# Kernel tuning notes

Measured on AMD Instinct MI355X. Metric: run time of the kernel, lower is better.

The kernel has to match this reference:

```python
import jax, jax.numpy as jnp
import numpy as np

B, T = 128, 2048
E, OUT, HID = 8, 32, 64          # num_experts, kan_out_features, gru_hidden_dim
GRID_SIZE, ORDER = 5, 3          # standard efficient-kan defaults
KCOEF = GRID_SIZE + ORDER        # B-spline basis functions per input feature


def make_grid():
    # extended knot grid on [-1, 1], length GRID_SIZE + 2*ORDER + 1
    h = 2.0 / GRID_SIZE
    return jnp.arange(-ORDER, GRID_SIZE + ORDER + 1, dtype=jnp.float32) * h - 1.0


def b_splines(x, grid):
    # x: [..., in_features] -> [..., in_features, KCOEF] via Cox-de Boor recursion
    x = x[..., None]
    b = ((x >= grid[:-1]) & (x < grid[1:])).astype(x.dtype)
    for k in range(1, ORDER + 1):
        left = (x - grid[:-(k + 1)]) / (grid[k:-1] - grid[:-(k + 1)])
        right = (grid[k + 1:] - x) / (grid[k + 1:] - grid[1:-k])
        b = left * b[..., :-1] + right * b[..., 1:]
    return b


def kan_moe(x, gate_w, gate_b, base_w, spline_w, grid):
    # x: [B,T,in=1]; dense softmax-gated mixture of KANLinear experts
    gate = jax.nn.softmax(x @ gate_w + gate_b, axis=-1)                 # [B,T,E]
    base_out = jnp.einsum('bti,eoi->bteo', jax.nn.silu(x), base_w)      # [B,T,E,OUT]
    bs = b_splines(x, grid).reshape(x.shape[0], x.shape[1], -1)         # [B,T,in*KCOEF]
    spline_out = jnp.einsum('btk,eok->bteo', bs, spline_w)              # [B,T,E,OUT]
    return jnp.einsum('bte,bteo->bto', gate, base_out + spline_out)     # [B,T,OUT]


def gru(x, w_ih, w_hh, b_ih, b_hh):
    # PyTorch GRU convention: gates ordered (r, z, n); batch_first semantics
    xp = jnp.einsum('btf,gf->btg', x, w_ih) + b_ih                      # [B,T,3H]

    def step(h, xt):
        hp = h @ w_hh.T + b_hh
        xr, xz, xn = jnp.split(xt, 3, axis=-1)
        hr, hz, hn = jnp.split(hp, 3, axis=-1)
        r = jax.nn.sigmoid(xr + hr)
        z = jax.nn.sigmoid(xz + hz)
        n = jnp.tanh(xn + r * hn)
        h = (1.0 - z) * n + z * h
        return h, h

    h0 = jnp.zeros((x.shape[0], HID), x.dtype)
    _, hs = jax.lax.scan(step, h0, jnp.swapaxes(xp, 0, 1))
    return jnp.swapaxes(hs, 0, 1)                                       # [B,T,H]


def setup_inputs() -> dict:
    key = jax.random.key(0)
    ks = jax.random.split(key, 12)
    def n(k, shape, scale=0.1):
        return jax.random.normal(k, shape, jnp.float32) * scale
    return {
        'a': jax.random.normal(ks[0], (B, T, 1), jnp.float32),
        'd': jax.random.normal(ks[1], (B, T, 1), jnp.float32),
        'gate_w_a': n(ks[2], (1, E)), 'gate_b_a': jnp.zeros((E,), jnp.float32),
        'base_w_a': n(ks[3], (E, OUT, 1)), 'spline_w_a': n(ks[4], (E, OUT, KCOEF)),
        'gate_w_d': n(ks[5], (1, E)), 'gate_b_d': jnp.zeros((E,), jnp.float32),
        'base_w_d': n(ks[6], (E, OUT, 1)), 'spline_w_d': n(ks[7], (E, OUT, KCOEF)),
        'conv_w': n(ks[8], (OUT, OUT, 5)), 'conv_b': jnp.zeros((OUT,), jnp.float32),
        'w_ih': n(ks[9], (3 * HID, OUT)), 'w_hh': n(ks[10], (3 * HID, HID)),
        'b_ih': jnp.zeros((3 * HID,), jnp.float32), 'b_hh': jnp.zeros((3 * HID,), jnp.float32),
    }


def reference(a, d, gate_w_a, gate_b_a, base_w_a, spline_w_a,
              gate_w_d, gate_b_d, base_w_d, spline_w_d,
              conv_w, conv_b, w_ih, w_hh, b_ih, b_hh):
    grid = make_grid()
    fa = kan_moe(a, gate_w_a, gate_b_a, base_w_a, spline_w_a, grid)     # trend features
    fd = kan_moe(d, gate_w_d, gate_b_d, base_w_d, spline_w_d, grid)     # residual features
    # TemporalBlock: permute -> Conv1d(padding='same') -> ReLU -> permute back
    xc = jnp.swapaxes(fa, 1, 2)                                         # [B,C,T]
    yc = jax.lax.conv_general_dilated(
        xc, conv_w, (1,), 'SAME', dimension_numbers=('NCH', 'OIH', 'NCH')
    ) + conv_b[None, :, None]
    trend = jnp.swapaxes(jax.nn.relu(yc), 1, 2)                         # [B,T,OUT]
    ctx = gru(fd, w_ih, w_hh, b_ih, b_hh)                               # [B,T,HID]
    # dropout is identity in eval mode
    return jnp.concatenate([trend, ctx], axis=-1)                       # [B,T,OUT+HID]
```

## Files before the change

kernel.cpp:

```cpp
#include <hip/hip_runtime.h>
#include <cstdint>

typedef _Float16 half2_t __attribute__((ext_vector_type(2)));

#define B_   128
#define T_   2048
#define E_   8
#define OUT_ 32
#define HID_ 64
#define KC_  8
#define TILE_A 128
#define NSEG 4
#define SEGT (T_ / NSEG)
#define WUPC 4
#define CH_  32

__device__ __forceinline__ float frcp(float x) { return __builtin_amdgcn_rcpf(x); }
__device__ __forceinline__ float exp2_(float x) {
#if __has_builtin(__builtin_amdgcn_exp2f)
  return __builtin_amdgcn_exp2f(x);
#else
  return exp2f(x);
#endif
}
__device__ __forceinline__ float fsig(float x) { return frcp(1.0f + __expf(-x)); }

__device__ __forceinline__ float fdot2_(half2_t a, half2_t b, float c) {
#if __has_builtin(__builtin_amdgcn_fdot2)
  return __builtin_amdgcn_fdot2(a, b, c, false);
#else
  return fmaf((float)a.x, (float)b.x, fmaf((float)a.y, (float)b.y, c));
#endif
}

__device__ __forceinline__ half2_t u2h2(unsigned u) {
  return __builtin_bit_cast(half2_t, u);
}
__device__ __forceinline__ half2_t packh2(float a, float b) {
  half2_t h; h.x = (_Float16)a; h.y = (_Float16)b; return h;
}
__device__ __forceinline__ float rlanef(float v, int i) {
  return __int_as_float(__builtin_amdgcn_readlane(__float_as_int(v), i));
}
__device__ __forceinline__ unsigned rlaneu(unsigned v, int i) {
  return (unsigned)__builtin_amdgcn_readlane((int)v, i);
}

#define NLOG2E  (-1.4426950408889634f)
#define N2LOG2E (-2.8853900817779268f)

__device__ __forceinline__ void kan_scalars(float x, const float* gwr, const float* gbr,
                                            float& silu, float* gate, float* bs) {
  silu = x * fsig(x);
  float le[E_];
  float m = -1e30f;
#pragma unroll
  for (int e = 0; e < E_; ++e) { le[e] = fmaf(x, gwr[e], gbr[e]); m = fmaxf(m, le[e]); }
  float s = 0.f;
#pragma unroll
  for (int e = 0; e < E_; ++e) { gate[e] = __expf(le[e] - m); s += gate[e]; }
  float inv = frcp(s);
#pragma unroll
  for (int e = 0; e < E_; ++e) gate[e] *= inv;
  float g[12];
#pragma unroll
  for (int i = 0; i < 12; ++i) g[i] = (float)(i - 3) * 0.4f - 1.0f;
  float bb[11];
#pragma unroll
  for (int i = 0; i < 11; ++i) bb[i] = (x >= g[i] && x < g[i + 1]) ? 1.0f : 0.0f;
#pragma unroll
  for (int k = 1; k <= 3; ++k) {
#pragma unroll
    for (int i = 0; i < 11 - k; ++i) {
      const float dl = 1.0f / (g[i + k] - g[i]);
      const float dr = 1.0f / (g[i + k + 1] - g[i + 1]);
      float left  = (x - g[i]) * dl;
      float right = (g[i + k + 1] - x) * dr;
      bb[i] = left * bb[i] + right * bb[i + 1];
    }
  }
#pragma unroll
  for (int i = 0; i < KC_; ++i) bs[i] = bb[i];
}

__global__ __launch_bounds__(256, 1) void fused3_kernel(
    const float* __restrict__ a, const float* __restrict__ d,
    const float* __restrict__ gwa, const float* __restrict__ gba,
    const float* __restrict__ bwa, const float* __restrict__ swa,
    const float* __restrict__ gwd, const float* __restrict__ gbd,
    const float* __restrict__ bwd, const float* __restrict__ swd,
    const float* __restrict__ cw, const float* __restrict__ cb,
    const float* __restrict__ wih_g, const float* __restrict__ whh_g,
    const float* __restrict__ bih_g, const float* __restrict__ bhh_g,
    float* __restrict__ out)
{
  __shared__ __align__(16) char smem_[47360];
  const int tid = threadIdx.x;

  if (blockIdx.x < NSEG * B_) {
    auto xqc = (uint2 (*)[CH_][64])smem_;
    auto hbc = (unsigned short*)(smem_ + 32768);

    const int bid = (int)blockIdx.x;
    const int b = bid & (B_ - 1);
    const int seg = bid >> 7;
    const int tstart = (seg == 0) ? 0 : (seg * SEGT - WUPC * CH_);
    const int wup = (seg == 0) ? 0 : WUPC;
    const int nch = ((seg == 0) ? SEGT : (SEGT + WUPC * CH_)) / CH_;
    const int w = tid >> 6;
    const int role = (w - (bid & 3)) & 3;
    const int ln = tid & 63;
    const size_t db = (size_t)b * T_;
    float* outrow = out + db * 96 + 32;
    const uint4* hq4 = (const uint4*)hbc;

    half2_t whhp[3][32];
    float bhh3[3];
    uint4 u0, u1, u2, u3, u4, u5, u6, u7;
    if (role == 0) {
#pragma unroll
      for (int g3 = 0; g3 < 3; ++g3) {
        const float sc = (g3 == 2) ? N2LOG2E : NLOG2E;
        const int g = g3 * 64 + ln;
#pragma unroll
        for (int i = 0; i < 64; i += 4) {
          const float4 v = *(const float4*)&whh_g[(size_t)g * 64 + i];
          whhp[g3][i / 2]     = packh2(v.x * sc, v.y * sc);
          whhp[g3][i / 2 + 1] = packh2(v.z * sc, v.w * sc);
        }
        bhh3[g3] = bhh_g[g] * sc;
      }
      hbc[ln] = __builtin_bit_cast(unsigned short, (_Float16)0.0f);
      asm volatile("" ::: "memory");
      u0 = hq4[0]; u1 = hq4[1]; u2 = hq4[2]; u3 = hq4[3];
      u4 = hq4[4]; u5 = hq4[5]; u6 = hq4[6]; u7 = hq4[7];
    }

    float A_[E_];
    half2_t Beh[E_][4];
    float bihr = 0.f;
    float gwrd[E_], gbrd[E_];
    const int p3 = (role >= 1) ? (role - 1) : 0;
    if (role >= 1) {
      const float sc = (p3 == 2) ? N2LOG2E : NLOG2E;
      const int g = p3 * 64 + ln;
      float wihr[32];
#pragma unroll
      for (int i = 0; i < 32; i += 4) {
        float4 v = *(const float4*)&wih_g[(size_t)g * 32 + i];
        wihr[i] = v.x * sc; wihr[i + 1] = v.y * sc;
        wihr[i + 2] = v.z * sc; wihr[i + 3] = v.w * sc;
      }
      bihr = bih_g[g] * sc;
#pragma unroll
      for (int e = 0; e < E_; ++e) { gwrd[e] = gwd[e]; gbrd[e] = gbd[e]; }
#pragma unroll
      for (int e = 0; e < E_; ++e) {
        float acc = 0.f;
#pragma unroll 4
        for (int c = 0; c < 32; c += 4) {
          const float4 bv = *(const float4*)&bwd[e * OUT_ + c];
          acc = fmaf(wihr[c], bv.x, acc);
          acc = fmaf(wihr[c + 1], bv.y, acc);
          acc = fmaf(wihr[c + 2], bv.z, acc);
          acc = fmaf(wihr[c + 3], bv.w, acc);
        }
        A_[e] = acc;
      }
#pragma unroll
      for (int e = 0; e < E_; ++e) {
        float bk[KC_];
#pragma unroll
        for (int k = 0; k < KC_; ++k) bk[k] = 0.f;
#pragma unroll 4
        for (int c = 0; c < 32; ++c) {
          const float4 s0 = *(const float4*)&swd[(e * OUT_ + c) * KC_ + 0];
          const float4 s1 = *(const float4*)&swd[(e * OUT_ + c) * KC_ + 4];
          const float wc = wihr[c];
          bk[0] = fmaf(wc, s0.x, bk[0]); bk[1] = fmaf(wc, s0.y, bk[1]);
          bk[2] = fmaf(wc, s0.z, bk[2]); bk[3] = fmaf(wc, s0.w, bk[3]);
          bk[4] = fmaf(wc, s1.x, bk[4]); bk[5] = fmaf(wc, s1.y, bk[5]);
          bk[6] = fmaf(wc, s1.z, bk[6]); bk[7] = fmaf(wc, s1.w, bk[7]);
        }
#pragma unroll
        for (int q = 0; q < 4; ++q) Beh[e][q] = packh2(bk[2 * q], bk[2 * q + 1]);
      }
    }

    float h = 0.0f;

    for (int ic = 0; ic <= nch; ++ic) {
      if (role >= 1 && ic < nch) {
        const int p = ic & 1;
        float my_silu, my_gate[E_], my_bs[KC_];
        {
          const float x = d[db + tstart + ic * CH_ + (ln & (CH_ - 1))];
          kan_scalars(x, gwrd, gbrd, my_silu, my_gate, my_bs);
        }
        unsigned my_bsp[4];
#pragma unroll
        for (int q = 0; q < 4; ++q)
          my_bsp[q] = __builtin_bit_cast(unsigned, packh2(my_bs[2 * q], my_bs[2 * q + 1]));

#pragma unroll 2
        for (int t = 0; t < CH_; ++t) {
          const float silu_t = rlanef(my_silu, t);
          const float gv0 = rlanef(my_gate[0], t), gv1 = rlanef(my_gate[1], t);
          const float gv2 = rlanef(my_gate[2], t), gv3 = rlanef(my_gate[3], t);
          const float gv4 = rlanef(my_gate[4], t), gv5 = rlanef(my_gate[5], t);
          const float gv6 = rlanef(my_gate[6], t), gv7 = rlanef(my_gate[7], t);
          const half2_t b0 = u2h2(rlaneu(my_bsp[0], t));
          const half2_t b1 = u2h2(rlaneu(my_bsp[1], t));
          const half2_t b2 = u2h2(rlaneu(my_bsp[2], t));
          const half2_t b3 = u2h2(rlaneu(my_bsp[3], t));
          float acc = bihr;
          {
            float in0 = silu_t * A_[0];
            in0 = fdot2_(b0, Beh[0][0], in0); in0 = fdot2_(b1, Beh[0][1], in0);
            in0 = fdot2_(b2, Beh[0][2], in0); in0 = fdot2_(b3, Beh[0][3], in0);
            acc = fmaf(gv0, in0, acc);
            float in1 = silu_t * A_[1];
            in1 = fdot2_(b0, Beh[1][0], in1); in1 = fdot2_(b1, Beh[1][1], in1);
            in1 = fdot2_(b2, Beh[1][2], in1); in1 = fdot2_(b3, Beh[1][3], in1);
            acc = fmaf(gv1, in1, acc);
            float in2 = silu_t * A_[2];
            in2 = fdot2_(b0, Beh[2][0], in2); in2 = fdot2_(b1, Beh[2][1], in2);
            in2 = fdot2_(b2, Beh[2][2], in2); in2 = fdot2_(b3, Beh[2][3], in2);
            acc = fmaf(gv2, in2, acc);
            float in3 = silu_t * A_[3];
            in3 = fdot2_(b0, Beh[3][0], in3); in3 = fdot2_(b1, Beh[3][1], in3);
            in3 = fdot2_(b2, Beh[3][2], in3); in3 = fdot2_(b3, Beh[3][3], in3);
            acc = fmaf(gv3, in3, acc);
            float in4 = silu_t * A_[4];
            in4 = fdot2_(b0, Beh[4][0], in4); in4 = fdot2_(b1, Beh[4][1], in4);
            in4 = fdot2_(b2, Beh[4][2], in4); in4 = fdot2_(b3, Beh[4][3], in4);
            acc = fmaf(gv4, in4, acc);
            float in5 = silu_t * A_[5];
            in5 = fdot2_(b0, Beh[5][0], in5); in5 = fdot2_(b1, Beh[5][1], in5);
            in5 = fdot2_(b2, Beh[5][2], in5); in5 = fdot2_(b3, Beh[5][3], in5);
            acc = fmaf(gv5, in5, acc);
            float in6 = silu_t * A_[6];
            in6 = fdot2_(b0, Beh[6][0], in6); in6 = fdot2_(b1, Beh[6][1], in6);
            in6 = fdot2_(b2, Beh[6][2], in6); in6 = fdot2_(b3, Beh[6][3], in6);
            acc = fmaf(gv6, in6, acc);
            float in7 = silu_t * A_[7];
            in7 = fdot2_(b0, Beh[7][0], in7); in7 = fdot2_(b1, Beh[7][1], in7);
            in7 = fdot2_(b2, Beh[7][2], in7); in7 = fdot2_(b3, Beh[7][3], in7);
            acc = fmaf(gv7, in7, acc);
          }
          ((_Float16*)&xqc[p][t][ln])[p3] = (_Float16)acc;
        }
      }

      if (role == 0 && ic >= 1) {
        const int jc = ic - 1;
        const int p = jc & 1;
        const int tb = tstart + jc * CH_;
        const bool do_store = (jc >= wup);
        const uint2 rc0 = xqc[p][0][ln];
        half2_t rz0 = u2h2(rc0.x);
        float xr = (float)rz0.x, xz = (float)rz0.y;
        float xn = (float)__builtin_bit_cast(half2_t, rc0.y).x;
        __builtin_amdgcn_s_setprio(1);
#pragma unroll 1
        for (int s = 0; s < CH_; ++s) {
          float ar0 = bhh3[0], ar1 = xr, ar2 = 0.f, ar3 = 0.f;
          float az0 = bhh3[1], az1 = xz, az2 = 0.f, az3 = 0.f;
          float an0 = bhh3[2], an1 = 0.f, an2 = 0.f, an3 = 0.f;
          {
            const half2_t q0 = u2h2(u0.x), q1 = u2h2(u0.y), q2 = u2h2(u0.z), q3 = u2h2(u0.w);
            ar0 = fdot2_(whhp[0][0], q0, ar0); ar1 = fdot2_(whhp[0][1], q1, ar1);
            ar2 = fdot2_(whhp[0][2], q2, ar2); ar3 = fdot2_(whhp[0][3], q3, ar3);
            az0 = fdot2_(whhp[1][0], q0, az0); az1 = fdot2_(whhp[1][1], q1, az1);
            az2 = fdot2_(whhp[1][2], q2, az2); az3 = fdot2_(whhp[1][3], q3, az3);
            an0 = fdot2_(whhp[2][0], q0, an0); an1 = fdot2_(whhp[2][1], q1, an1);
            an2 = fdot2_(whhp[2][2], q2, an2); an3 = fdot2_(whhp[2][3], q3, an3);
          }
          {
            const half2_t q0 = u2h2(u1.x), q1 = u2h2(u1.y), q2 = u2h2(u1.z), q3 = u2h2(u1.w);
            ar0 = fdot2_(whhp[0][4], q0, ar0); ar1 = fdot2_(whhp[0][5], q1, ar1);
            ar2 = fdot2_(whhp[0][6], q2, ar2); ar3 = fdot2_(whhp[0][7], q3, ar3);
            az0 = fdot2_(whhp[1][4], q0, az0); az1 = fdot2_(whhp[1][5], q1, az1);
            az2 = fdot2_(whhp[1][6], q2, az2); az3 = fdot2_(whhp[1][7], q3, az3);
            an0 = fdot2_(whhp[2][4], q0, an0); an1 = fdot2_(whhp[2][5], q1, an1);
            an2 = fdot2_(whhp[2][6], q2, an2); an3 = fdot2_(whhp[2][7], q3, an3);
          }
          {
            const half2_t q0 = u2h2(u2.x), q1 = u2h2(u2.y), q2 = u2h2(u2.z), q3 = u2h2(u2.w);
            ar0 = fdot2_(whhp[0][8], q0, ar0); ar1 = fdot2_(whhp[0][9], q1, ar1);
            ar2 = fdot2_(whhp[0][10], q2, ar2); ar3 = fdot2_(whhp[0][11], q3, ar3);
            az0 = fdot2_(whhp[1][8], q0, az0); az1 = fdot2_(whhp[1][9], q1, az1);
            az2 = fdot2_(whhp[1][10], q2, az2); az3 = fdot2_(whhp[1][11], q3, az3);
            an0 = fdot2_(whhp[2][8], q0, an0); an1 = fdot2_(whhp[2][9], q1, an1);
            an2 = fdot2_(whhp[2][10], q2, an2); an3 = fdot2_(whhp[2][11], q3, an3);
          }
          {
            const half2_t q0 = u2h2(u3.x), q1 = u2h2(u3.y), q2 = u2h2(u3.z), q3 = u2h2(u3.w);
            ar0 = fdot2_(whhp[0][12], q0, ar0); ar1 = fdot2_(whhp[0][13], q1, ar1);
            ar2 = fdot2_(whhp[0][14], q2, ar2); ar3 = fdot2_(whhp[0][15], q3, ar3);
            az0 = fdot2_(whhp[1][12], q0, az0); az1 = fdot2_(whhp[1][13], q1, az1);
            az2 = fdot2_(whhp[1][14], q2, az2); az3 = fdot2_(whhp[1][15], q3, az3);
            an0 = fdot2_(whhp[2][12], q0, an0); an1 = fdot2_(whhp[2][13], q1, an1);
            an2 = fdot2_(whhp[2][14], q2, an2); an3 = fdot2_(whhp[2][15], q3, an3);
          }
          {
            const half2_t q0 = u2h2(u4.x), q1 = u2h2(u4.y), q2 = u2h2(u4.z), q3 = u2h2(u4.w);
            ar0 = fdot2_(whhp[0][16], q0, ar0); ar1 = fdot2_(whhp[0][17], q1, ar1);
            ar2 = fdot2_(whhp[0][18], q2, ar2); ar3 = fdot2_(whhp[0][19], q3, ar3);
            az0 = fdot2_(whhp[1][16], q0, az0); az1 = fdot2_(whhp[1][17], q1, az1);
            az2 = fdot2_(whhp[1][18], q2, az2); az3 = fdot2_(whhp[1][19], q3, az3);
            an0 = fdot2_(whhp[2][16], q0, an0); an1 = fdot2_(whhp[2][17], q1, an1);
            an2 = fdot2_(whhp[2][18], q2, an2); an3 = fdot2_(whhp[2][19], q3, an3);
          }
          {
            const half2_t q0 = u2h2(u5.x), q1 = u2h2(u5.y), q2 = u2h2(u5.z), q3 = u2h2(u5.w);
            ar0 = fdot2_(whhp[0][20], q0, ar0); ar1 = fdot2_(whhp[0][21], q1, ar1);
            ar2 = fdot2_(whhp[0][22], q2, ar2); ar3 = fdot2_(whhp[0][23], q3, ar3);
            az0 = fdot2_(whhp[1][20], q0, az0); az1 = fdot2_(whhp[1][21], q1, az1);
            az2 = fdot2_(whhp[1][22], q2, az2); az3 = fdot2_(whhp[1][23], q3, az3);
            an0 = fdot2_(whhp[2][20], q0, an0); an1 = fdot2_(whhp[2][21], q1, an1);
            an2 = fdot2_(whhp[2][22], q2, an2); an3 = fdot2_(whhp[2][23], q3, an3);
          }
          {
            const half2_t q0 = u2h2(u6.x), q1 = u2h2(u6.y), q2 = u2h2(u6.z), q3 = u2h2(u6.w);
            ar0 = fdot2_(whhp[0][24], q0, ar0); ar1 = fdot2_(whhp[0][25], q1, ar1);
            ar2 = fdot2_(whhp[0][26], q2, ar2); ar3 = fdot2_(whhp[0][27], q3, ar3);
            az0 = fdot2_(whhp[1][24], q0, az0); az1 = fdot2_(whhp[1][25], q1, az1);
            az2 = fdot2_(whhp[1][26], q2, az2); az3 = fdot2_(whhp[1][27], q3, az3);
            an0 = fdot2_(whhp[2][24], q0, an0); an1 = fdot2_(whhp[2][25], q1, an1);
            an2 = fdot2_(whhp[2][26], q2, an2); an3 = fdot2_(whhp[2][27], q3, an3);
          }
          {
            const half2_t q0 = u2h2(u7.x), q1 = u2h2(u7.y), q2 = u2h2(u7.z), q3 = u2h2(u7.w);
            ar0 = fdot2_(whhp[0][28], q0, ar0); ar1 = fdot2_(whhp[0][29], q1, ar1);
            ar2 = fdot2_(whhp[0][30], q2, ar2); ar3 = fdot2_(whhp[0][31], q3, ar3);
            az0 = fdot2_(whhp[1][28], q0, az0); az1 = fdot2_(whhp[1][29], q1, az1);
            az2 = fdot2_(whhp[1][30], q2, az2); az3 = fdot2_(whhp[1][31], q3, az3);
            an0 = fdot2_(whhp[2][28], q0, an0); an1 = fdot2_(whhp[2][29], q1, an1);
            an2 = fdot2_(whhp[2][30], q2, an2); an3 = fdot2_(whhp[2][31], q3, an3);
          }
          const float hr = (ar0 + ar1) + (ar2 + ar3);
          const float hz = (az0 + az1) + (az2 + az3);
          const float hn = (an0 + an1) + (an2 + an3);
          const float r = frcp(1.0f + exp2_(hr));
          const float z = frcp(1.0f + exp2_(hz));
          const float tn = frcp(1.0f + exp2_(fmaf(r, hn, xn)));
          const float n = fmaf(2.0f, tn, -1.0f);
          h = n + z * (h - n);
          hbc[ln] = __builtin_bit_cast(unsigned short, (_Float16)h);
          asm volatile("" ::: "memory");
          const int sn = (s + 1) & (CH_ - 1);
          const uint2 rcn = xqc[p][sn][ln];
          u0 = hq4[0]; u1 = hq4[1]; u2 = hq4[2]; u3 = hq4[3];
          u4 = hq4[4]; u5 = hq4[5]; u6 = hq4[6]; u7 = hq4[7];
          asm volatile("" ::: "memory");
          if (do_store) outrow[(size_t)(tb + s) * 96 + ln] = h;
          const half2_t rzh = u2h2(rcn.x);
          xr = (float)rzh.x; xz = (float)rzh.y;
          xn = (float)__builtin_bit_cast(half2_t, rcn.y).x;
        }
        __builtin_amdgcn_s_setprio(0);
      }
      __syncthreads();
    }
  } else {
    auto fa  = (float (*)[136])smem_;
    auto cwl = (float (*)[161])(smem_ + 17408);
    auto swl = (float (*)[OUT_][KC_])(smem_ + 38016);
    auto bwl = (float (*)[OUT_])(smem_ + 46208);
    float* gwl = (float*)(smem_ + 47232);
    float* gbl = (float*)(smem_ + 47264);

    for (int i = tid; i < OUT_ * OUT_ * 5; i += 256) cwl[i / 160][i % 160] = cw[i];
    for (int i = tid; i < E_ * OUT_ * KC_; i += 256) ((float*)swl)[i] = swa[i];
    for (int i = tid; i < E_ * OUT_; i += 256) ((float*)bwl)[i] = bwa[i];
    if (tid < E_) { gwl[tid] = gwa[tid]; gbl[tid] = gba[tid]; }
    __syncthreads();

    const int cid = blockIdx.x - NSEG * B_;
#pragma unroll 1
    for (int it = 0; it < 16; ++it) {
      const int gt = cid + it * 128;
      const int bb = gt >> 4;
      const int t0 = (gt & 15) * TILE_A;
      if (tid < TILE_A + 4) {
        const int i = tid;
        const int t = t0 + i - 2;
        const bool inr = (t >= 0) && (t < T_);
        const float x = inr ? a[(size_t)bb * T_ + t] : 0.0f;
        float gwr[E_], gbr[E_];
#pragma unroll
        for (int e = 0; e < E_; ++e) { gwr[e] = gwl[e]; gbr[e] = gbl[e]; }
        float silu, gate[E_], bs[KC_];
        kan_scalars(x, gwr, gbr, silu, gate, bs);
#pragma unroll 4
        for (int cc = 0; cc < OUT_; ++cc) {
          float accb = 0.f, accs = 0.f;
#pragma unroll
          for (int e = 0; e < E_; ++e) {
            accb = fmaf(gate[e], bwl[e][cc], accb);
            const float4 s0 = *(const float4*)&swl[e][cc][0];
            const float4 s1 = *(const float4*)&swl[e][cc][4];
            float dot = bs[0]*s0.x + bs[1]*s0.y + bs[2]*s0.z + bs[3]*s0.w
                      + bs[4]*s1.x + bs[5]*s1.y + bs[6]*s1.z + bs[7]*s1.w;
            accs = fmaf(gate[e], dot, accs);
          }
          fa[cc][i] = inr ? fmaf(silu, accb, accs) : 0.0f;
        }
      }
      __syncthreads();
      {
        const int o = tid & 31;
        const int grp = tid >> 5;
        const float bias = cb[o];
        float acc[16];
#pragma unroll
        for (int q = 0; q < 16; ++q) acc[q] = bias;
        for (int c = 0; c < OUT_; ++c) {
          float col[20];
#pragma unroll
          for (int q = 0; q < 5; ++q)
            *(float4*)&col[q * 4] = *(const float4*)&fa[c][grp * 16 + q * 4];
#pragma unroll
          for (int jj = 0; jj < 5; ++jj) {
            const float wv = cwl[o][c * 5 + jj];
#pragma unroll
            for (int q = 0; q < 16; ++q) acc[q] = fmaf(col[q + jj], wv, acc[q]);
          }
        }
#pragma unroll
        for (int q = 0; q < 16; ++q) {
          const int t = t0 + grp * 16 + q;
          out[((size_t)bb * T_ + t) * 96 + o] = fmaxf(acc[q], 0.0f);
        }
      }
      __syncthreads();
    }
  }
}

extern "C" void kernel_launch(void* const* d_in, const int* in_sizes, int n_in,
                              void* d_out, int out_size, void* d_ws, size_t ws_size,
                              hipStream_t stream) {
  (void)in_sizes; (void)n_in; (void)out_size; (void)d_ws; (void)ws_size;
  const float* a        = (const float*)d_in[0];
  const float* d        = (const float*)d_in[1];
  const float* gate_w_a = (const float*)d_in[2];
  const float* gate_b_a = (const float*)d_in[3];
  const float* base_w_a = (const float*)d_in[4];
  const float* spln_w_a = (const float*)d_in[5];
  const float* gate_w_d = (const float*)d_in[6];
  const float* gate_b_d = (const float*)d_in[7];
  const float* base_w_d = (const float*)d_in[8];
  const float* spln_w_d = (const float*)d_in[9];
  const float* conv_w   = (const float*)d_in[10];
  const float* conv_b   = (const float*)d_in[11];
  const float* w_ih     = (const float*)d_in[12];
  const float* w_hh     = (const float*)d_in[13];
  const float* b_ih     = (const float*)d_in[14];
  const float* b_hh     = (const float*)d_in[15];
  float* out = (float*)d_out;

  fused3_kernel<<<NSEG * B_ + B_, 256, 0, stream>>>(
      a, d, gate_w_a, gate_b_a, base_w_a, spln_w_a,
      gate_w_d, gate_b_d, base_w_d, spln_w_d,
      conv_w, conv_b, w_ih, w_hh, b_ih, b_hh, out);
}
```

Baseline: 640.3 us.

## Interleave four batch rows per GRU wave and run conv in same blocks

Each block now advances the GRU recurrence for four batch rows at once inside the single recurrent wave, using chunks of 16 steps and a 128-step warmup over four time segments. The grid shrinks to 128 blocks, and every block runs the trend conv work after its GRU loop instead of relying on separate conv blocks. The aim is to hide the per-step latency of the recurrence with independent work from the other rows. It also avoids the multiple rounds of blocks the old 640-block grid needed with one block per CU. The cost is more work per step on the serial path, fewer active CUs, and the conv now sits serially behind the GRU in each block.

After: 1.164 ms. 81.8% more time.

```diff
diff --git a/kernel.cpp b/kernel.cpp
--- a/kernel.cpp
+++ b/kernel.cpp
@@ -11,9 +11,10 @@
 #define KC_  8
 #define TILE_A 128
 #define NSEG 4
-#define SEGT (T_ / NSEG)
-#define WUPC 4
-#define CH_  32
+#define CH_  16
+#define NCHB 38
+#define WUPC_ 8
+#define SEGOUT 480
 
 __device__ __forceinline__ float frcp(float x) { return __builtin_amdgcn_rcpf(x); }
 __device__ __forceinline__ float exp2_(float x) {
@@ -83,7 +84,7 @@
   for (int i = 0; i < KC_; ++i) bs[i] = bb[i];
 }
 
-__global__ __launch_bounds__(256, 1) void fused3_kernel(
+__global__ __launch_bounds__(256, 1) void fused8_kernel(
     const float* __restrict__ a, const float* __restrict__ d,
     const float* __restrict__ gwa, const float* __restrict__ gba,
     const float* __restrict__ bwa, const float* __restrict__ swa,
@@ -94,276 +95,237 @@
     const float* __restrict__ bih_g, const float* __restrict__ bhh_g,
     float* __restrict__ out)
 {
-  __shared__ __align__(16) char smem_[47360];
+  __shared__ __align__(16) char smem_[49664];
   const int tid = threadIdx.x;
 
-  if (blockIdx.x < NSEG * B_) {
-    auto xqc = (uint2 (*)[CH_][64])smem_;
-    auto hbc = (unsigned short*)(smem_ + 32768);
-
-    const int bid = (int)blockIdx.x;
-    const int b = bid & (B_ - 1);
-    const int seg = bid >> 7;
-    const int tstart = (seg == 0) ? 0 : (seg * SEGT - WUPC * CH_);
-    const int wup = (seg == 0) ? 0 : WUPC;
-    const int nch = ((seg == 0) ? SEGT : (SEGT + WUPC * CH_)) / CH_;
-    const int w = tid >> 6;
-    const int role = (w - (bid & 3)) & 3;
-    const int ln = tid & 63;
-    const size_t db = (size_t)b * T_;
-    float* outrow = out + db * 96 + 32;
-    const uint4* hq4 = (const uint4*)hbc;
-
-    half2_t whhp[3][32];
-    float bhh3[3];
-    uint4 u0, u1, u2, u3, u4, u5, u6, u7;
-    if (role == 0) {
-#pragma unroll
-      for (int g3 = 0; g3 < 3; ++g3) {
-        const float sc = (g3 == 2) ? N2LOG2E : NLOG2E;
-        const int g = g3 * 64 + ln;
-#pragma unroll
-        for (int i = 0; i < 64; i += 4) {
-          const float4 v = *(const float4*)&whh_g[(size_t)g * 64 + i];
-          whhp[g3][i / 2]     = packh2(v.x * sc, v.y * sc);
-          whhp[g3][i / 2 + 1] = packh2(v.z * sc, v.w * sc);
-        }
-        bhh3[g3] = bhh_g[g] * sc;
-      }
-      hbc[ln] = __builtin_bit_cast(unsigned short, (_Float16)0.0f);
-      asm volatile("" ::: "memory");
-      u0 = hq4[0]; u1 = hq4[1]; u2 = hq4[2]; u3 = hq4[3];
-      u4 = hq4[4]; u5 = hq4[5]; u6 = hq4[6]; u7 = hq4[7];
-    }
-
-    float A_[E_];
-    half2_t Beh[E_][4];
-    float bihr = 0.f;
-    float gwrd[E_], gbrd[E_];
-    const int p3 = (role >= 1) ? (role - 1) : 0;
-    if (role >= 1) {
-      const float sc = (p3 == 2) ? N2LOG2E : NLOG2E;
-      const int g = p3 * 64 + ln;
-      float wihr[32];
-#pragma unroll
-      for (int i = 0; i < 32; i += 4) {
-        float4 v = *(const float4*)&wih_g[(size_t)g * 32 + i];
-        wihr[i] = v.x * sc; wihr[i + 1] = v.y * sc;
-        wihr[i + 2] = v.z * sc; wihr[i + 3] = v.w * sc;
-      }
-      bihr = bih_g[g] * sc;
-#pragma unroll
-      for (int e = 0; e < E_; ++e) { gwrd[e] = gwd[e]; gbrd[e] = gbd[e]; }
-#pragma unroll
-      for (int e = 0; e < E_; ++e) {
-        float acc = 0.f;
+  auto xqrz = (unsigned (*)[2][CH_][64])smem_;
+  auto xqn  = (_Float16 (*)[2][CH_][64])(smem_ + 32768);
+  auto hbc  = (unsigned short (*)[64])(smem_ + 49152);
+
+  const int bid = (int)blockIdx.x;
+  const int seg = bid >> 5;
+  const int quad = bid & 31;
+  const int w = tid >> 6;
+  const int ln = tid & 63;
+  const int tstart = seg * SEGOUT;
+  const int wup = (seg == 0) ? 0 : WUPC_;
+  const int p3 = (w >= 1) ? (w - 1) : 0;
+
+  half2_t whhp[3][32];
+  float bhh3[3];
+  if (w == 0) {
+#pragma unroll
+    for (int g3 = 0; g3 < 3; ++g3) {
+      const float sc = (g3 == 2) ? N2LOG2E : NLOG2E;
+      const int g = g3 * 64 + ln;
+#pragma unroll
+      for (int i = 0; i < 64; i += 4) {
+        const float4 v = *(const float4*)&whh_g[(size_t)g * 64 + i];
+        whhp[g3][i / 2]     = packh2(v.x * sc, v.y * sc);
+        whhp[g3][i / 2 + 1] = packh2(v.z * sc, v.w * sc);
+      }
+      bhh3[g3] = bhh_g[g] * sc;
+    }
+#pragma unroll
+    for (int q = 0; q < 4; ++q)
+      hbc[q][ln] = __builtin_bit_cast(unsigned short, (_Float16)0.0f);
+    asm volatile("" ::: "memory");
+  }
+
+  float A_[E_];
+  half2_t Beh[E_][4];
+  float bihr = 0.f;
+  float gwrd[E_], gbrd[E_];
+  if (w >= 1) {
+    const float sc = (p3 == 2) ? N2LOG2E : NLOG2E;
+    const int g = p3 * 64 + ln;
+    float wihr[32];
+#pragma unroll
+    for (int i = 0; i < 32; i += 4) {
+      float4 v = *(const float4*)&wih_g[(size_t)g * 32 + i];
+      wihr[i] = v.x * sc; wihr[i + 1] = v.y * sc;
+      wihr[i + 2] = v.z * sc; wihr[i + 3] = v.w * sc;
+    }
+    bihr = bih_g[g] * sc;
+#pragma unroll
+    for (int e = 0; e < E_; ++e) { gwrd[e] = gwd[e]; gbrd[e] = gbd[e]; }
+#pragma unroll
+    for (int e = 0; e < E_; ++e) {
+      float acc = 0.f;
 #pragma unroll 4
-        for (int c = 0; c < 32; c += 4) {
-          const float4 bv = *(const float4*)&bwd[e * OUT_ + c];
-          acc = fmaf(wihr[c], bv.x, acc);
-          acc = fmaf(wihr[c + 1], bv.y, acc);
-          acc = fmaf(wihr[c + 2], bv.z, acc);
-          acc = fmaf(wihr[c + 3], bv.w, acc);
-        }
-        A_[e] = acc;
-      }
-#pragma unroll
-      for (int e = 0; e < E_; ++e) {
-        float bk[KC_];
-#pragma unroll
-        for (int k = 0; k < KC_; ++k) bk[k] = 0.f;
+      for (int c = 0; c < 32; c += 4) {
+        const float4 bv = *(const float4*)&bwd[e * OUT_ + c];
+        acc = fmaf(wihr[c], bv.x, acc);
+        acc = fmaf(wihr[c + 1], bv.y, acc);
+        acc = fmaf(wihr[c + 2], bv.z, acc);
+        acc = fmaf(wihr[c + 3], bv.w, acc);
+      }
+      A_[e] = acc;
+    }
+#pragma unroll
+    for (int e = 0; e < E_; ++e) {
+      float bk[KC_];
+#pragma unroll
+      for (int k = 0; k < KC_; ++k) bk[k] = 0.f;
 #pragma unroll 4
-        for (int c = 0; c < 32; ++c) {
-          const float4 s0 = *(const float4*)&swd[(e * OUT_ + c) * KC_ + 0];
-          const float4 s1 = *(const float4*)&swd[(e * OUT_ + c) * KC_ + 4];
-          const float wc = wihr[c];
-          bk[0] = fmaf(wc, s0.x, bk[0]); bk[1] = fmaf(wc, s0.y, bk[1]);
-          bk[2] = fmaf(wc, s0.z, bk[2]); bk[3] = fmaf(wc, s0.w, bk[3]);
-          bk[4] = fmaf(wc, s1.x, bk[4]); bk[5] = fmaf(wc, s1.y, bk[5]);
-          bk[6] = fmaf(wc, s1.z, bk[6]); bk[7] = fmaf(wc, s1.w, bk[7]);
-        }
-#pragma unroll
-        for (int q = 0; q < 4; ++q) Beh[e][q] = packh2(bk[2 * q], bk[2 * q + 1]);
-      }
-    }
-
-    float h = 0.0f;
-
-    for (int ic = 0; ic <= nch; ++ic) {
-      if (role >= 1 && ic < nch) {
-        const int p = ic & 1;
-        float my_silu, my_gate[E_], my_bs[KC_];
+      for (int c = 0; c < 32; ++c) {
+        const float4 s0 = *(const float4*)&swd[(e * OUT_ + c) * KC_ + 0];
+        const float4 s1 = *(const float4*)&swd[(e * OUT_ + c) * KC_ + 4];
+        const float wc = wihr[c];
+        bk[0] = fmaf(wc, s0.x, bk[0]); bk[1] = fmaf(wc, s0.y, bk[1]);
+        bk[2] = fmaf(wc, s0.z, bk[2]); bk[3] = fmaf(wc, s0.w, bk[3]);
+        bk[4] = fmaf(wc, s1.x, bk[4]); bk[5] = fmaf(wc, s1.y, bk[5]);
+        bk[6] = fmaf(wc, s1.z, bk[6]); bk[7] = fmaf(wc, s1.w, bk[7]);
+      }
+#pragma unroll
+      for (int q = 0; q < 4; ++q) Beh[e][q] = packh2(bk[2 * q], bk[2 * q + 1]);
+    }
+  }
+
+  float hq[4] = {0.f, 0.f, 0.f, 0.f};
+
+  for (int ic = 0; ic <= NCHB; ++ic) {
+    if (w >= 1 && ic < NCHB) {
+      const int p = ic & 1;
+      float my_silu, my_gate[E_], my_bs[KC_];
+      {
+        const int u = ln >> 4;
+        const size_t dbu = (size_t)(quad * 4 + u) * T_;
+        const float x = d[dbu + tstart + ic * CH_ + (ln & 15)];
+        kan_scalars(x, gwrd, gbrd, my_silu, my_gate, my_bs);
+      }
+      unsigned my_bsp[4];
+#pragma unroll
+      for (int q = 0; q < 4; ++q)
+        my_bsp[q] = __builtin_bit_cast(unsigned, packh2(my_bs[2 * q], my_bs[2 * q + 1]));
+
+#pragma unroll 2
+      for (int it = 0; it < 64; ++it) {
+        const int uu = it >> 4, tt = it & 15;
+        const float silu_t = rlanef(my_silu, it);
+        const float gv0 = rlanef(my_gate[0], it), gv1 = rlanef(my_gate[1], it);
+        const float gv2 = rlanef(my_gate[2], it), gv3 = rlanef(my_gate[3], it);
+        const float gv4 = rlanef(my_gate[4], it), gv5 = rlanef(my_gate[5], it);
+        const float gv6 = rlanef(my_gate[6], it), gv7 = rlanef(my_gate[7], it);
+        const half2_t b0 = u2h2(rlaneu(my_bsp[0], it));
+        const half2_t b1 = u2h2(rlaneu(my_bsp[1], it));
+        const half2_t b2 = u2h2(rlaneu(my_bsp[2], it));
+        const half2_t b3 = u2h2(rlaneu(my_bsp[3], it));
+        float acc = bihr;
         {
-          const float x = d[db + tstart + ic * CH_ + (ln & (CH_ - 1))];
-          kan_scalars(x, gwrd, gbrd, my_silu, my_gate, my_bs);
-        }
-        unsigned my_bsp[4];
-#pragma unroll
-        for (int q = 0; q < 4; ++q)
-          my_bsp[q] = __builtin_bit_cast(unsigned, packh2(my_bs[2 * q], my_bs[2 * q + 1]));
-
-#pragma unroll 2
-        for (int t = 0; t < CH_; ++t) {
-          const float silu_t = rlanef(my_silu, t);
-          const float gv0 = rlanef(my_gate[0], t), gv1 = rlanef(my_gate[1], t);
-          const float gv2 = rlanef(my_gate[2], t), gv3 = rlanef(my_gate[3], t);
-          const float gv4 = rlanef(my_gate[4], t), gv5 = rlanef(my_gate[5], t);
-          const float gv6 = rlanef(my_gate[6], t), gv7 = rlanef(my_gate[7], t);
-          const half2_t b0 = u2h2(rlaneu(my_bsp[0], t));
-          const half2_t b1 = u2h2(rlaneu(my_bsp[1], t));
-          const half2_t b2 = u2h2(rlaneu(my_bsp[2], t));
-          const half2_t b3 = u2h2(rlaneu(my_bsp[3], t));
-          float acc = bihr;
-          {
-            float in0 = silu_t * A_[0];
-            in0 = fdot2_(b0, Beh[0][0], in0); in0 = fdot2_(b1, Beh[0][1], in0);
-            in0 = fdot2_(b2, Beh[0][2], in0); in0 = fdot2_(b3, Beh[0][3], in0);
-            acc = fmaf(gv0, in0, acc);
-            float in1 = silu_t * A_[1];
-            in1 = fdot2_(b0, Beh[1][0], in1); in1 = fdot2_(b1, Beh[1][1], in1);
-            in1 = fdot2_(b2, Beh[1][2], in1); in1 = fdot2_(b3, Beh[1][3], in1);
-            acc = fmaf(gv1, in1, acc);
-            float in2 = silu_t * A_[2];
-            in2 = fdot2_(b0, Beh[2][0], in2); in2 = fdot2_(b1, Beh[2][1], in2);
-            in2 = fdot2_(b2, Beh[2][2], in2); in2 = fdot2_(b3, Beh[2][3], in2);
-            acc = fmaf(gv2, in2, acc);
-            float in3 = silu_t * A_[3];
-            in3 = fdot2_(b0, Beh[3][0], in3); in3 = fdot2_(b1, Beh[3][1], in3);
-            in3 = fdot2_(b2, Beh[3][2], in3); in3 = fdot2_(b3, Beh[3][3], in3);
-            acc = fmaf(gv3, in3, acc);
-            float in4 = silu_t * A_[4];
-            in4 = fdot2_(b0, Beh[4][0], in4); in4 = fdot2_(b1, Beh[4][1], in4);
-            in4 = fdot2_(b2, Beh[4][2], in4); in4 = fdot2_(b3, Beh[4][3], in4);
-            acc = fmaf(gv4, in4, acc);
-            float in5 = silu_t * A_[5];
-            in5 = fdot2_(b0, Beh[5][0], in5); in5 = fdot2_(b1, Beh[5][1], in5);
-            in5 = fdot2_(b2, Beh[5][2], in5); in5 = fdot2_(b3, Beh[5][3], in5);
-            acc = fmaf(gv5, in5, acc);
-            float in6 = silu_t * A_[6];
-            in6 = fdot2_(b0, Beh[6][0], in6); in6 = fdot2_(b1, Beh[6][1], in6);
-            in6 = fdot2_(b2, Beh[6][2], in6); in6 = fdot2_(b3, Beh[6][3], in6);
-            acc = fmaf(gv6, in6, acc);
-            float in7 = silu_t * A_[7];
-            in7 = fdot2_(b0, Beh[7][0], in7); in7 = fdot2_(b1, Beh[7][1], in7);
-            in7 = fdot2_(b2, Beh[7][2], in7); in7 = fdot2_(b3, Beh[7][3], in7);
-            acc = fmaf(gv7, in7, acc);
+          float in0 = silu_t * A_[0];
+          in0 = fdot2_(b0, Beh[0][0], in0); in0 = fdot2_(b1, Beh[0][1], in0);
+          in0 = fdot2_(b2, Beh[0][2], in0); in0 = fdot2_(b3, Beh[0][3], in0);
+          acc = fmaf(gv0, in0, acc);
+          float in1 = silu_t * A_[1];
+          in1 = fdot2_(b0, Beh[1][0], in1); in1 = fdot2_(b1, Beh[1][1], in1);
+          in1 = fdot2_(b2, Beh[1][2], in1); in1 = fdot2_(b3, Beh[1][3], in1);
+          acc = fmaf(gv1, in1, acc);
+          float in2 = silu_t * A_[2];
+          in2 = fdot2_(b0, Beh[2][0], in2); in2 = fdot2_(b1, Beh[2][1], in2);
+          in2 = fdot2_(b2, Beh[2][2], in2); in2 = fdot2_(b3, Beh[2][3], in2);
+          acc = fmaf(gv2, in2, acc);
+          float in3 = silu_t * A_[3];
+          in3 = fdot2_(b0, Beh[3][0], in3); in3 = fdot2_(b1, Beh[3][1], in3);
+          in3 = fdot2_(b2, Beh[3][2], in3); in3 = fdot2_(b3, Beh[3][3], in3);
+          acc = fmaf(gv3, in3, acc);
+          float in4 = silu_t * A_[4];
+          in4 = fdot2_(b0, Beh[4][0], in4); in4 = fdot2_(b1, Beh[4][1], in4);
+          in4 = fdot2_(b2, Beh[4][2], in4); in4 = fdot2_(b3, Beh[4][3], in4);
+          acc = fmaf(gv4, in4, acc);
+          float in5 = silu_t * A_[5];
+          in5 = fdot2_(b0, Beh[5][0], in5); in5 = fdot2_(b1, Beh[5][1], in5);
+          in5 = fdot2_(b2, Beh[5][2], in5); in5 = fdot2_(b3, Beh[5][3], in5);
+          acc = fmaf(gv5, in5, acc);
+          float in6 = silu_t * A_[6];
+          in6 = fdot2_(b0, Beh[6][0], in6); in6 = fdot2_(b1, Beh[6][1], in6);
+          in6 = fdot2_(b2, Beh[6][2], in6); in6 = fdot2_(b3, Beh[6][3], in6);
+          acc = fmaf(gv6, in6, acc);
+          float in7 = silu_t * A_[7];
+          in7 = fdot2_(b0, Beh[7][0], in7); in7 = fdot2_(b1, Beh[7][1], in7);
+          in7 = fdot2_(b2, Beh[7][2], in7); in7 = fdot2_(b3, Beh[7][3], in7);
+          acc = fmaf(gv7, in7, acc);
+        }
+        if (p3 < 2) ((_Float16*)&xqrz[uu][p][tt][ln])[p3] = (_Float16)acc;
+        else        xqn[uu][p][tt][ln] = (_Float16)acc;
+      }
+    }
+
+    if (w == 0 && ic >= 1) {
+      const int jc = ic - 1;
+      const int p = jc & 1;
+      const int tb = tstart + jc * CH_;
+      const bool do_store = (jc >= wup);
+      float xr[4], xz[4], xn[4];
+#pragma unroll
+      for (int q = 0; q < 4; ++q) {
+        const half2_t rz0 = u2h2(xqrz[q][p][0][ln]);
+        xr[q] = (float)rz0.x; xz[q] = (float)rz0.y;
+        xn[q] = (float)xqn[q][p][0][ln];
+      }
+      __builtin_amdgcn_s_setprio(1);
+#pragma unroll 1
+      for (int s = 0; s < CH_; ++s) {
+        float hr[4], hz[4], hn_[4];
+#pragma unroll
+        for (int q = 0; q < 4; ++q) {
+          const uint4* hq4 = (const uint4*)&hbc[q][0];
+          uint4 v[8];
+#pragma unroll
+          for (int k = 0; k < 8; ++k) v[k] = hq4[k];
+          float a0 = bhh3[0], a1 = xr[q], a2 = 0.f, a3 = 0.f;
+          float z0 = bhh3[1], z1 = xz[q], z2 = 0.f, z3 = 0.f;
+          float c0 = bhh3[2], c1 = 0.f, c2 = 0.f, c3 = 0.f;
+#pragma unroll
+          for (int k = 0; k < 8; ++k) {
+            const half2_t q0 = u2h2(v[k].x), q1 = u2h2(v[k].y);
+            const half2_t q2 = u2h2(v[k].z), q3 = u2h2(v[k].w);
+            a0 = fdot2_(whhp[0][4 * k + 0], q0, a0);
+            a1 = fdot2_(whhp[0][4 * k + 1], q1, a1);
+            a2 = fdot2_(whhp[0][4 * k + 2], q2, a2);
+            a3 = fdot2_(whhp[0][4 * k + 3], q3, a3);
+            z0 = fdot2_(whhp[1][4 * k + 0], q0, z0);
+            z1 = fdot2_(whhp[1][4 * k + 1], q1, z1);
+            z2 = fdot2_(whhp[1][4 * k + 2], q2, z2);
+            z3 = fdot2_(whhp[1][4 * k + 3], q3, z3);
+            c0 = fdot2_(whhp[2][4 * k + 0], q0, c0);
+            c1 = fdot2_(whhp[2][4 * k + 1], q1, c1);
+            c2 = fdot2_(whhp[2][4 * k + 2], q2, c2);
+            c3 = fdot2_(whhp[2][4 * k + 3], q3, c3);
           }
-          ((_Float16*)&xqc[p][t][ln])[p3] = (_Float16)acc;
-        }
-      }
-
-      if (role == 0 && ic >= 1) {
-        const int jc = ic - 1;
-        const int p = jc & 1;
-        const int tb = tstart + jc * CH_;
-        const bool do_store = (jc >= wup);
-        const uint2 rc0 = xqc[p][0][ln];
-        half2_t rz0 = u2h2(rc0.x);
-        float xr = (float)rz0.x, xz = (float)rz0.y;
-        float xn = (float)__builtin_bit_cast(half2_t, rc0.y).x;
-        __builtin_amdgcn_s_setprio(1);
-#pragma unroll 1
-        for (int s = 0; s < CH_; ++s) {
-          float ar0 = bhh3[0], ar1 = xr, ar2 = 0.f, ar3 = 0.f;
-          float az0 = bhh3[1], az1 = xz, az2 = 0.f, az3 = 0.f;
-          float an0 = bhh3[2], an1 = 0.f, an2 = 0.f, an3 = 0.f;
-          {
-            const half2_t q0 = u2h2(u0.x), q1 = u2h2(u0.y), q2 = u2h2(u0.z), q3 = u2h2(u0.w);
-            ar0 = fdot2_(whhp[0][0], q0, ar0); ar1 = fdot2_(whhp[0][1], q1, ar1);
-            ar2 = fdot2_(whhp[0][2], q2, ar2); ar3 = fdot2_(whhp[0][3], q3, ar3);
-            az0 = fdot2_(whhp[1][0], q0, az0); az1 = fdot2_(whhp[1][1], q1, az1);
-            az2 = fdot2_(whhp[1][2], q2, az2); az3 = fdot2_(whhp[1][3], q3, az3);
-            an0 = fdot2_(whhp[2][0], q0, an0); an1 = fdot2_(whhp[2][1], q1, an1);
-            an2 = fdot2_(whhp[2][2], q2, an2); an3 = fdot2_(whhp[2][3], q3, an3);
+          hr[q] = (a0 + a1) + (a2 + a3);
+          hz[q] = (z0 + z1) + (z2 + z3);
+          hn_[q] = (c0 + c1) + (c2 + c3);
+        }
+#pragma unroll
+        for (int q = 0; q < 4; ++q) {
+          const float r = frcp(1.0f + exp2_(hr[q]));
+          const float z = frcp(1.0f + exp2_(hz[q]));
+          const float tn = frcp(1.0f + exp2_(fmaf(r, hn_[q], xn[q])));
+          const float n = fmaf(2.0f, tn, -1.0f);
+          hq[q] = n + z * (hq[q] - n);
+          hbc[q][ln] = __builtin_bit_cast(unsigned short, (_Float16)hq[q]);
+        }
+        asm volatile("" ::: "memory");
+        const int sn = (s + 1) & (CH_ - 1);
+#pragma unroll
+        for (int q = 0; q < 4; ++q) {
+          const unsigned rzn = xqrz[q][p][sn][ln];
+          const _Float16 xnn = xqn[q][p][sn][ln];
+          if (do_store) {
+            const size_t dbu = (size_t)(quad * 4 + q) * T_;
+            out[(dbu + tb + s) * 96 + 32 + ln] = hq[q];
           }
-          {
-            const half2_t q0 = u2h2(u1.x), q1 = u2h2(u1.y), q2 = u2h2(u1.z), q3 = u2h2(u1.w);
-            ar0 = fdot2_(whhp[0][4], q0, ar0); ar1 = fdot2_(whhp[0][5], q1, ar1);
-            ar2 = fdot2_(whhp[0][6], q2, ar2); ar3 = fdot2_(whhp[0][7], q3, ar3);
-            az0 = fdot2_(whhp[1][4], q0, az0); az1 = fdot2_(whhp[1][5], q1, az1);
-            az2 = fdot2_(whhp[1][6], q2, az2); az3 = fdot2_(whhp[1][7], q3, az3);
-            an0 = fdot2_(whhp[2][4], q0, an0); an1 = fdot2_(whhp[2][5], q1, an1);
-            an2 = fdot2_(whhp[2][6], q2, an2); an3 = fdot2_(whhp[2][7], q3, an3);
-          }
-          {
-            const half2_t q0 = u2h2(u2.x), q1 = u2h2(u2.y), q2 = u2h2(u2.z), q3 = u2h2(u2.w);
-            ar0 = fdot2_(whhp[0][8], q0, ar0); ar1 = fdot2_(whhp[0][9], q1, ar1);
-            ar2 = fdot2_(whhp[0][10], q2, ar2); ar3 = fdot2_(whhp[0][11], q3, ar3);
-            az0 = fdot2_(whhp[1][8], q0, az0); az1 = fdot2_(whhp[1][9], q1, az1);
-            az2 = fdot2_(whhp[1][10], q2, az2); az3 = fdot2_(whhp[1][11], q3, az3);
-            an0 = fdot2_(whhp[2][8], q0, an0); an1 = fdot2_(whhp[2][9], q1, an1);
-            an2 = fdot2_(whhp[2][10], q2, an2); an3 = fdot2_(whhp[2][11], q3, an3);
-          }
-          {
-            const half2_t q0 = u2h2(u3.x), q1 = u2h2(u3.y), q2 = u2h2(u3.z), q3 = u2h2(u3.w);
-            ar0 = fdot2_(whhp[0][12], q0, ar0); ar1 = fdot2_(whhp[0][13], q1, ar1);
-            ar2 = fdot2_(whhp[0][14], q2, ar2); ar3 = fdot2_(whhp[0][15], q3, ar3);
-            az0 = fdot2_(whhp[1][12], q0, az0); az1 = fdot2_(whhp[1][13], q1, az1);
-            az2 = fdot2_(whhp[1][14], q2, az2); az3 = fdot2_(whhp[1][15], q3, az3);
-            an0 = fdot2_(whhp[2][12], q0, an0); an1 = fdot2_(whhp[2][13], q1, an1);
-            an2 = fdot2_(whhp[2][14], q2, an2); an3 = fdot2_(whhp[2][15], q3, an3);
-          }
-          {
-            const half2_t q0 = u2h2(u4.x), q1 = u2h2(u4.y), q2 = u2h2(u4.z), q3 = u2h2(u4.w);
-            ar0 = fdot2_(whhp[0][16], q0, ar0); ar1 = fdot2_(whhp[0][17], q1, ar1);
-            ar2 = fdot2_(whhp[0][18], q2, ar2); ar3 = fdot2_(whhp[0][19], q3, ar3);
-            az0 = fdot2_(whhp[1][16], q0, az0); az1 = fdot2_(whhp[1][17], q1, az1);
-            az2 = fdot2_(whhp[1][18], q2, az2); az3 = fdot2_(whhp[1][19], q3, az3);
-            an0 = fdot2_(whhp[2][16], q0, an0); an1 = fdot2_(whhp[2][17], q1, an1);
-            an2 = fdot2_(whhp[2][18], q2, an2); an3 = fdot2_(whhp[2][19], q3, an3);
-          }
-          {
-            const half2_t q0 = u2h2(u5.x), q1 = u2h2(u5.y), q2 = u2h2(u5.z), q3 = u2h2(u5.w);
-            ar0 = fdot2_(whhp[0][20], q0, ar0); ar1 = fdot2_(whhp[0][21], q1, ar1);
-            ar2 = fdot2_(whhp[0][22], q2, ar2); ar3 = fdot2_(whhp[0][23], q3, ar3);
-            az0 = fdot2_(whhp[1][20], q0, az0); az1 = fdot2_(whhp[1][21], q1, az1);
-            az2 = fdot2_(whhp[1][22], q2, az2); az3 = fdot2_(whhp[1][23], q3, az3);
-            an0 = fdot2_(whhp[2][20], q0, an0); an1 = fdot2_(whhp[2][21], q1, an1);
-            an2 = fdot2_(whhp[2][22], q2, an2); an3 = fdot2_(whhp[2][23], q3, an3);
-          }
-          {
-            const half2_t q0 = u2h2(u6.x), q1 = u2h2(u6.y), q2 = u2h2(u6.z), q3 = u2h2(u6.w);
-            ar0 = fdot2_(whhp[0][24], q0, ar0); ar1 = fdot2_(whhp[0][25], q1, ar1);
-            ar2 = fdot2_(whhp[0][26], q2, ar2); ar3 = fdot2_(whhp[0][27], q3, ar3);
-            az0 = fdot2_(whhp[1][24], q0, az0); az1 = fdot2_(whhp[1][25], q1, az1);
-            az2 = fdot2_(whhp[1][26], q2, az2); az3 = fdot2_(whhp[1][27], q3, az3);
-            an0 = fdot2_(whhp[2][24], q0, an0); an1 = fdot2_(whhp[2][25], q1, an1);
-            an2 = fdot2_(whhp[2][26], q2, an2); an3 = fdot2_(whhp[2][27], q3, an3);
-          }
-          {
-            const half2_t q0 = u2h2(u7.x), q1 = u2h2(u7.y), q2 = u2h2(u7.z), q3 = u2h2(u7.w);
-            ar0 = fdot2_(whhp[0][28], q0, ar0); ar1 = fdot2_(whhp[0][29], q1, ar1);
-            ar2 = fdot2_(whhp[0][30], q2, ar2); ar3 = fdot2_(whhp[0][31], q3, ar3);
-            az0 = fdot2_(whhp[1][28], q0, az0); az1 = fdot2_(whhp[1][29], q1, az1);
-            az2 = fdot2_(whhp[1][30], q2, az2); az3 = fdot2_(whhp[1][31], q3, az3);
-            an0 = fdot2_(whhp[2][28], q0, an0); an1 = fdot2_(whhp[2][29], q1, an1);
-            an2 = fdot2_(whhp[2][30], q2, an2); an3 = fdot2_(whhp[2][31], q3, an3);
-          }
-          const float hr = (ar0 + ar1) + (ar2 + ar3);
-          const float hz = (az0 + az1) + (az2 + az3);
-          const float hn = (an0 + an1) + (an2 + an3);
-          const float r = frcp(1.0f + exp2_(hr));
-          const float z = frcp(1.0f + exp2_(hz));
-          const float tn = frcp(1.0f + exp2_(fmaf(r, hn, xn)));
-          const float n = fmaf(2.0f, tn, -1.0f);
-          h = n + z * (h - n);
-          hbc[ln] = __builtin_bit_cast(unsigned short, (_Float16)h);
-          asm volatile("" ::: "memory");
-          const int sn = (s + 1) & (CH_ - 1);
-          const uint2 rcn = xqc[p][sn][ln];
-          u0 = hq4[0]; u1 = hq4[1]; u2 = hq4[2]; u3 = hq4[3];
-          u4 = hq4[4]; u5 = hq4[5]; u6 = hq4[6]; u7 = hq4[7];
-          asm volatile("" ::: "memory");
-          if (do_store) outrow[(size_t)(tb + s) * 96 + ln] = h;
-          const half2_t rzh = u2h2(rcn.x);
-          xr = (float)rzh.x; xz = (float)rzh.y;
-          xn = (float)__builtin_bit_cast(half2_t, rcn.y).x;
-        }
-        __builtin_amdgcn_s_setprio(0);
-      }
-      __syncthreads();
-    }
-  } else {
+          const half2_t rzh = u2h2(rzn);
+          xr[q] = (float)rzh.x; xz[q] = (float)rzh.y; xn[q] = (float)xnn;
+        }
+      }
+      __builtin_amdgcn_s_setprio(0);
+    }
+    __syncthreads();
+  }
+
+  {
     auto fa  = (float (*)[136])smem_;
     auto cwl = (float (*)[161])(smem_ + 17408);
     auto swl = (float (*)[OUT_][KC_])(smem_ + 38016);
@@ -377,10 +339,9 @@
     if (tid < E_) { gwl[tid] = gwa[tid]; gbl[tid] = gba[tid]; }
     __syncthreads();
 
-    const int cid = blockIdx.x - NSEG * B_;
 #pragma unroll 1
     for (int it = 0; it < 16; ++it) {
-      const int gt = cid + it * 128;
+      const int gt = bid + it * 128;
       const int bb = gt >> 4;
       const int t0 = (gt & 15) * TILE_A;
       if (tid < TILE_A + 4) {
@@ -461,7 +422,7 @@
   const float* b_hh     = (const float*)d_in[15];
   float* out = (float*)d_out;
 
-  fused3_kernel<<<NSEG * B_ + B_, 256, 0, stream>>>(
+  fused8_kernel<<<B_, 256, 0, stream>>>(
       a, d, gate_w_a, gate_b_a, base_w_a, spln_w_a,
       gate_w_d, gate_b_d, base_w_d, spln_w_d,
       conv_w, conv_b, w_ih, w_hh, b_ih, b_hh, out);
```
